# Optimization experiments

Measured on AMD Instinct MI355X. Metric: run time of the kernel, lower is better.

The kernel has to match this reference:

```python
import jax, jax.numpy as jnp
import numpy as np

B, S, E, H = 2, 2048, 2048, 16
D = E // H  # head_dim = 128
EPS = 1e-5


def setup_inputs() -> dict:
    key = jax.random.key(0)
    ks = jax.random.split(key, 16)
    s_e = 1.0 / np.sqrt(E)
    s_f = 1.0 / np.sqrt(4 * E)
    return {
        "x": jax.random.normal(ks[0], (B, S, E), jnp.float32),
        "ln1_w": jnp.ones((E,), jnp.float32) + 0.01 * jax.random.normal(ks[1], (E,)),
        "ln1_b": 0.01 * jax.random.normal(ks[2], (E,)),
        "wq": s_e * jax.random.normal(ks[3], (E, E), jnp.float32),
        "wk": s_e * jax.random.normal(ks[4], (E, E), jnp.float32),
        "wv": s_e * jax.random.normal(ks[5], (E, E), jnp.float32),
        "wo": s_e * jax.random.normal(ks[6], (E, E), jnp.float32),
        "bo": 0.01 * jax.random.normal(ks[7], (E,)),
        "ln2_w": jnp.ones((E,), jnp.float32) + 0.01 * jax.random.normal(ks[8], (E,)),
        "ln2_b": 0.01 * jax.random.normal(ks[9], (E,)),
        "w1": s_e * jax.random.normal(ks[10], (E, 4 * E), jnp.float32),
        "b1": 0.01 * jax.random.normal(ks[11], (4 * E,)),
        "w2": s_f * jax.random.normal(ks[12], (4 * E, E), jnp.float32),
        "b2": 0.01 * jax.random.normal(ks[13], (E,)),
    }


def _layernorm(x, w, b):
    mu = jnp.mean(x, axis=-1, keepdims=True)
    var = jnp.var(x, axis=-1, keepdims=True)
    return (x - mu) * jax.lax.rsqrt(var + EPS) * w + b


def _attention(x, wq, wk, wv, wo, bo):
    # x: [B,S,E] -> q,k,v: [B,H,S,D]
    def split(t):
        return t.reshape(B, S, H, D).transpose(0, 2, 1, 3)
    q = split(x @ wq)
    k = split(x @ wk)
    v = split(x @ wv)
    scores = jnp.einsum("bhqd,bhkd->bhqk", q, k)  # [B,H,S,S]
    causal = jnp.triu(jnp.ones((S, S), bool), k=1)
    scores = jnp.where(causal, -jnp.inf, scores)
    # NOTE: faithful to source -- scaling applied after masking, inside softmax arg
    attn = jax.nn.softmax(scores / np.sqrt(D), axis=-1)
    ctx = jnp.einsum("bhqk,bhkd->bhqd", attn, v)
    ctx = ctx.transpose(0, 2, 1, 3).reshape(B, S, E)
    return ctx @ wo + bo


def reference(x, ln1_w, ln1_b, wq, wk, wv, wo, bo, ln2_w, ln2_b, w1, b1, w2, b2):
    shortcut = x
    x1 = _layernorm(x, ln1_w, ln1_b)
    attn_out = _attention(x1, wq, wk, wv, wo, bo)
    a = attn_out + shortcut
    # NOTE: faithful to source quirk -- second shortcut is post-LN1 x1, not a
    y = _layernorm(a, ln2_w, ln2_b)
    y = jax.nn.gelu(y @ w1 + b1, approximate=False) @ w2 + b2
    return x1 + y
```

## Files before the change

### kernel.cpp

```cpp
#include <hip/hip_runtime.h>
#include <math.h>

typedef unsigned short u16;
typedef unsigned int u32;
typedef __attribute__((ext_vector_type(8))) short short8;
typedef __attribute__((ext_vector_type(4))) float f32x4;
typedef __attribute__((ext_vector_type(16))) float f32x16;
typedef __attribute__((ext_vector_type(4))) u32 u32x4;
typedef __attribute__((ext_vector_type(2))) u32 u32x2;

#define DEVFN static __device__ __forceinline__

DEVFN u16 f2bf(float x) {
  union { float f; u32 u; } v; v.f = x;
  u32 r = v.u + 0x7fffu + ((v.u >> 16) & 1u);
  return (u16)(r >> 16);
}
DEVFN float bf2f(u16 h) {
  union { u32 u; float f; } v; v.u = ((u32)h) << 16;
  return v.f;
}
DEVFN u32 packbf2(float a, float b) {
  return (u32)f2bf(a) | ((u32)f2bf(b) << 16);
}
DEVFN void gl2lds16(const u16* g, u16* l) {
  __builtin_amdgcn_global_load_lds(
      (const __attribute__((address_space(1))) u32*)g,
      (__attribute__((address_space(3))) u32*)l, 16, 0, 0);
}

__global__ __launch_bounds__(256) void tconv_k(const float* __restrict__ in,
                                               u16* __restrict__ out, int K, int N) {
  __shared__ float tile[32][33];
  int n0 = blockIdx.x << 5, k0 = blockIdx.y << 5;
  int tx = threadIdx.x & 31, ty = threadIdx.x >> 5;
#pragma unroll
  for (int i = 0; i < 32; i += 8)
    tile[ty + i][tx] = in[(long)(k0 + ty + i) * N + n0 + tx];
  __syncthreads();
#pragma unroll
  for (int i = 0; i < 32; i += 8)
    out[(long)(n0 + ty + i) * K + k0 + tx] = f2bf(tile[tx][ty + i]);
}

__global__ __launch_bounds__(256) void ln1_k(const float* __restrict__ x,
                                             const float* __restrict__ w,
                                             const float* __restrict__ b,
                                             float* __restrict__ y32,
                                             u16* __restrict__ y16) {
  long base = (long)blockIdx.x * 2048;
  int t = threadIdx.x;
  float4 v0 = ((const float4*)(x + base))[2 * t];
  float4 v1 = ((const float4*)(x + base))[2 * t + 1];
  float xv[8];
  *(float4*)xv = v0; *(float4*)(xv + 4) = v1;
  float s = 0.f, ss = 0.f;
#pragma unroll
  for (int i = 0; i < 8; ++i) { s += xv[i]; ss += xv[i] * xv[i]; }
#pragma unroll
  for (int m = 1; m < 64; m <<= 1) { s += __shfl_xor(s, m); ss += __shfl_xor(ss, m); }
  __shared__ float rs[4], rss[4];
  int wave = t >> 6;
  if ((t & 63) == 0) { rs[wave] = s; rss[wave] = ss; }
  __syncthreads();
  s = rs[0] + rs[1] + rs[2] + rs[3];
  ss = rss[0] + rss[1] + rss[2] + rss[3];
  float mean = s * (1.f / 2048.f);
  float var = ss * (1.f / 2048.f) - mean * mean;
  float inv = rsqrtf(var + 1e-5f);
  float wv[8], bv[8];
  *(float4*)wv = ((const float4*)w)[2 * t]; *(float4*)(wv + 4) = ((const float4*)w)[2 * t + 1];
  *(float4*)bv = ((const float4*)b)[2 * t]; *(float4*)(bv + 4) = ((const float4*)b)[2 * t + 1];
  float yv[8];
#pragma unroll
  for (int i = 0; i < 8; ++i) yv[i] = (xv[i] - mean) * inv * wv[i] + bv[i];
  ((float4*)(y32 + base))[2 * t] = *(float4*)yv;
  ((float4*)(y32 + base))[2 * t + 1] = *(float4*)(yv + 4);
  u32x4 ov;
#pragma unroll
  for (int i = 0; i < 4; ++i) ov[i] = packbf2(yv[2 * i], yv[2 * i + 1]);
  ((u32x4*)(y16 + base))[t] = ov;
}

__global__ __launch_bounds__(256) void ln2_k(const u16* __restrict__ a,
                                             const float* __restrict__ w,
                                             const float* __restrict__ b,
                                             u16* __restrict__ y) {
  long base = (long)blockIdx.x * 2048;
  int t = threadIdx.x;
  u32x4 pv = ((const u32x4*)(a + base))[t];
  float xv[8];
#pragma unroll
  for (int i = 0; i < 4; ++i) {
    xv[2 * i] = bf2f((u16)(pv[i] & 0xffffu));
    xv[2 * i + 1] = bf2f((u16)(pv[i] >> 16));
  }
  float s = 0.f, ss = 0.f;
#pragma unroll
  for (int i = 0; i < 8; ++i) { s += xv[i]; ss += xv[i] * xv[i]; }
#pragma unroll
  for (int m = 1; m < 64; m <<= 1) { s += __shfl_xor(s, m); ss += __shfl_xor(ss, m); }
  __shared__ float rs[4], rss[4];
  int wave = t >> 6;
  if ((t & 63) == 0) { rs[wave] = s; rss[wave] = ss; }
  __syncthreads();
  s = rs[0] + rs[1] + rs[2] + rs[3];
  ss = rss[0] + rss[1] + rss[2] + rss[3];
  float mean = s * (1.f / 2048.f);
  float var = ss * (1.f / 2048.f) - mean * mean;
  float inv = rsqrtf(var + 1e-5f);
  float wv[8], bv[8];
  *(float4*)wv = ((const float4*)w)[2 * t]; *(float4*)(wv + 4) = ((const float4*)w)[2 * t + 1];
  *(float4*)bv = ((const float4*)b)[2 * t]; *(float4*)(bv + 4) = ((const float4*)b)[2 * t + 1];
  u32x4 ov;
#pragma unroll
  for (int i = 0; i < 4; ++i) {
    float y0 = (xv[2 * i] - mean) * inv * wv[2 * i] + bv[2 * i];
    float y1 = (xv[2 * i + 1] - mean) * inv * wv[2 * i + 1] + bv[2 * i + 1];
    ov[i] = packbf2(y0, y1);
  }
  ((u32x4*)(y + base))[t] = ov;
}

#define VMW4() asm volatile("s_waitcnt vmcnt(4)" ::: "memory")
#define VMW2() asm volatile("s_waitcnt vmcnt(2)" ::: "memory")
#define VMW0() asm volatile("s_waitcnt vmcnt(0)" ::: "memory")
#define CFENCE() asm volatile("" ::: "memory")
#define BARRIER() do { CFENCE(); __builtin_amdgcn_s_barrier(); CFENCE(); } while (0)

template <int MODE, int IM>
__global__ __launch_bounds__(512, 2) void gemm8_k(const u16* __restrict__ A,
                                                  const u16* __restrict__ W,
                                                  void* __restrict__ outp,
                                                  const float* __restrict__ bias,
                                                  const float* __restrict__ resid,
                                                  int M, int N, int K) {
  constexpr int BM = IM * 32;
  constexpr int BN = 256;
  __shared__ __align__(16) u16 lds[2][(BM + BN) * 64];
  const int t = threadIdx.x, lane = t & 63, wave = t >> 6;
  const int g = lane >> 4, r16 = lane & 15;
  const int wm = wave >> 2, wn = wave & 3;
  const int nM = M / BM;
  const int nwg = gridDim.x * gridDim.y;
  const int orig = blockIdx.y * gridDim.x + blockIdx.x;
  const int sw = (nwg & 7) ? orig : ((orig & 7) * (nwg >> 3) + (orig >> 3));
  const long m0 = (long)(sw % nM) * BM, n0 = (long)(sw / nM) * BN;
  const int nt = K >> 6;
  const long Kl = K;

  auto stA = [&](int b, int half, int tile) {
#pragma unroll
    for (int q = 0; q < 2; ++q) {
      int rl = (wave * 2 + q) * 8 + (lane >> 3);
      int c = (lane & 7) ^ (rl & 7);
      gl2lds16(A + (m0 + half * 128 + rl) * Kl + ((long)tile << 6) + c * 8,
               &lds[b][half * 8192 + (wave * 2 + q) * 512]);
    }
  };
  auto stB = [&](int b, int half, int tile) {
#pragma unroll
    for (int q = 0; q < 2; ++q) {
      int rl = (wave * 2 + q) * 8 + (lane >> 3);
      int c = (lane & 7) ^ (rl & 7);
      gl2lds16(W + (n0 + half * 128 + rl) * Kl + ((long)tile << 6) + c * 8,
               &lds[b][BM * 64 + half * 8192 + (wave * 2 + q) * 512]);
    }
  };

  f32x4 acc[IM][4] = {};
  short8 af[4][2], bf[2][2];

#define LDAF(IH)                                                              \
  _Pragma("unroll") for (int ii2 = 0; ii2 < 4; ++ii2) {                       \
    int row = (((IH)*4 + ii2) * 2 + wm) * 16 + r16;                           \
    _Pragma("unroll") for (int kk = 0; kk < 2; ++kk)                          \
        af[ii2][kk] = *(const short8*)(&lds[cur][row * 64 +                   \
                                        (((kk << 2) | g) ^ (row & 7)) * 8]);  \
  }
#define LDBF(JH)                                                              \
  _Pragma("unroll") for (int jj2 = 0; jj2 < 2; ++jj2) {                       \
    int row = (((JH)*2 + jj2) * 4 + wn) * 16 + r16;                           \
    _Pragma("unroll") for (int kk = 0; kk < 2; ++kk)                          \
        bf[jj2][kk] = *(const short8*)(&lds[cur][BM * 64 + row * 64 +         \
                                        (((kk << 2) | g) ^ (row & 7)) * 8]);  \
  }
#define MFMA_PH(IH, JH)                                                       \
  __builtin_amdgcn_s_setprio(1);                                              \
  _Pragma("unroll") for (int ii2 = 0; ii2 < 4; ++ii2)                         \
      _Pragma("unroll") for (int jj2 = 0; jj2 < 2; ++jj2)                     \
          _Pragma("unroll") for (int kk = 0; kk < 2; ++kk)                    \
              acc[(IH)*4 + ii2][(JH)*2 + jj2] =                               \
                  __builtin_amdgcn_mfma_f32_16x16x32_bf16(                    \
                      af[ii2][kk], bf[jj2][kk],                               \
                      acc[(IH)*4 + ii2][(JH)*2 + jj2], 0, 0, 0);              \
  __builtin_amdgcn_s_setprio(0);

  if constexpr (IM == 8) {
    stA(0, 0, 0); stB(0, 0, 0); stB(0, 1, 0); stA(0, 1, 0);
    VMW4();
  } else {
    stA(0, 0, 0); stB(0, 0, 0); stB(0, 1, 0);
    VMW2();
  }
  BARRIER();

  for (int tt = 0; tt < nt; ++tt) {
    const int cur = tt & 1, nxt = cur ^ 1;
    const int ts = (tt + 1 < nt) ? tt + 1 : tt;
    if constexpr (IM == 8) {
      LDAF(0); LDBF(0);
      stA(nxt, 0, ts);
      MFMA_PH(0, 0);
      VMW4(); BARRIER();
      LDBF(1);
      stB(nxt, 0, ts);
      MFMA_PH(0, 1);
      VMW4(); BARRIER();
      LDAF(1); LDBF(0);
      stB(nxt, 1, ts);
      MFMA_PH(1, 0);
      BARRIER();
      LDBF(1);
      stA(nxt, 1, ts);
      MFMA_PH(1, 1);
      VMW4(); BARRIER();
    } else {
      LDAF(0); LDBF(0);
      stA(nxt, 0, ts); stB(nxt, 0, ts);
      MFMA_PH(0, 0);
      VMW4(); BARRIER();
      LDBF(1);
      stB(nxt, 1, ts);
      MFMA_PH(0, 1);
      VMW2(); BARRIER();
    }
  }
  VMW0();

  const long Nl = N;
#pragma unroll
  for (int ii = 0; ii < IM; ++ii) {
#pragma unroll
    for (int jj = 0; jj < 4; ++jj) {
#pragma unroll
      for (int r = 0; r < 4; ++r) {
        long mg = m0 + (ii * 2 + wm) * 16 + g * 4 + r;
        long ng = n0 + (jj * 4 + wn) * 16 + r16;
        float v = acc[ii][jj][r];
        if constexpr (MODE == 0 || MODE == 1) {
          long bb = mg >> 11, sq = mg & 2047;
          long hh = ng >> 7, dd = ng & 127;
          long idx = (MODE == 0) ? (((bb * 16 + hh) * 2048 + sq) * 128 + dd)
                                 : (((bb * 16 + hh) * 128 + dd) * 2048 + sq);
          ((u16*)outp)[idx] = f2bf(v);
        } else if constexpr (MODE == 2) {
          v += bias[ng] + resid[mg * Nl + ng];
          ((u16*)outp)[mg * Nl + ng] = f2bf(v);
        } else if constexpr (MODE == 3) {
          v += bias[ng];
          v = 0.5f * v * (1.0f + erff(v * 0.70710678118654752f));
          ((u16*)outp)[mg * Nl + ng] = f2bf(v);
        } else {
          v += bias[ng] + resid[mg * Nl + ng];
          ((float*)outp)[mg * Nl + ng] = v;
        }
      }
    }
  }
#undef LDAF
#undef LDBF
#undef MFMA_PH
}

__global__ __launch_bounds__(256, 2) void attn2_k(const u16* __restrict__ Qp,
                                                  const u16* __restrict__ Kp,
                                                  const u16* __restrict__ Vp,
                                                  u16* __restrict__ ctx) {
  __shared__ __align__(16) u16 KsL[2][64 * 128];
  __shared__ __align__(16) u16 VsL[2][128 * 64];
  const int qt = gridDim.x - 1 - blockIdx.x;
  const int bh = blockIdx.y;
  const int t = threadIdx.x, lane = t & 63, wave = t >> 6;
  const int l31 = lane & 31, hi = lane >> 5;
  const int q0 = qt * 128, qw0 = q0 + wave * 32;
  const int qg = qw0 + l31;
  const u16* Qh = Qp + (long)bh * 2048 * 128;
  const u16* Kh = Kp + (long)bh * 2048 * 128;
  const u16* Vh = Vp + (long)bh * 128 * 2048;
  const int nkt = qt * 2 + 2;
  const int ktmax = (qw0 + 31) >> 6;
  const float cs = 0.12753042923810058f;

  short8 qf[8];
#pragma unroll
  for (int ds = 0; ds < 8; ++ds)
    qf[ds] = *(const short8*)(Qh + (long)qg * 128 + ds * 16 + hi * 8);

  f32x16 O0 = {}, O1 = {}, O2 = {}, O3 = {};
  float m = -INFINITY, l = 0.f;

  auto stage = [&](int b, int kt) {
#pragma unroll
    for (int q = 0; q < 4; ++q) {
      int r = wave * 16 + q * 4 + (lane >> 4);
      int c = (lane & 15) ^ (r & 15);
      gl2lds16(Kh + ((long)kt * 64 + r) * 128 + c * 8,
               &KsL[b][(wave * 16 + q * 4) * 128]);
    }
#pragma unroll
    for (int q = 0; q < 4; ++q) {
      int r = wave * 32 + q * 8 + (lane >> 3);
      int c = (lane & 7) ^ (r & 7);
      gl2lds16(Vh + (long)r * 2048 + kt * 64 + c * 8,
               &VsL[b][(wave * 32 + q * 8) * 64]);
    }
  };

  stage(0, 0);
  VMW0(); BARRIER();

  for (int kt = 0; kt < nkt; ++kt) {
    const int cur = kt & 1;
    if (kt + 1 < nkt) stage(cur ^ 1, kt + 1);
    if (kt <= ktmax) {
      f32x16 S0 = {}, S1 = {};
      __builtin_amdgcn_s_setprio(1);
#pragma unroll
      for (int ds = 0; ds < 8; ++ds) {
        int c0 = ((ds * 2 + hi) ^ (l31 & 15)) * 8;
        short8 k0 = *(const short8*)(&KsL[cur][l31 * 128 + c0]);
        int r1 = 32 + l31;
        int c1 = ((ds * 2 + hi) ^ (r1 & 15)) * 8;
        short8 k1 = *(const short8*)(&KsL[cur][r1 * 128 + c1]);
        S0 = __builtin_amdgcn_mfma_f32_32x32x16_bf16(k0, qf[ds], S0, 0, 0, 0);
        S1 = __builtin_amdgcn_mfma_f32_32x32x16_bf16(k1, qf[ds], S1, 0, 0, 0);
      }
      __builtin_amdgcn_s_setprio(0);
      float p[32];
#pragma unroll
      for (int i = 0; i < 16; ++i) { p[i] = S0[i]; p[16 + i] = S1[i]; }
      if (kt * 64 + 63 > qw0) {
#pragma unroll
        for (int ks = 0; ks < 2; ++ks)
#pragma unroll
          for (int r = 0; r < 16; ++r) {
            int kg = kt * 64 + ks * 32 + (r & 3) + 8 * (r >> 2) + 4 * hi;
            if (kg > qg) p[ks * 16 + r] = -INFINITY;
          }
      }
      float tmax = p[0];
#pragma unroll
      for (int i = 1; i < 32; ++i) tmax = fmaxf(tmax, p[i]);
      tmax = fmaxf(tmax, __shfl_xor(tmax, 32));
      float mnew = fmaxf(m, tmax);
      float corr = __builtin_amdgcn_exp2f((m - mnew) * cs);
      float ls = 0.f;
#pragma unroll
      for (int i = 0; i < 32; ++i) {
        p[i] = __builtin_amdgcn_exp2f((p[i] - mnew) * cs);
        ls += p[i];
      }
      ls += __shfl_xor(ls, 32);
      l = l * corr + ls;
      m = mnew;
#pragma unroll
      for (int i = 0; i < 16; ++i) {
        O0[i] *= corr; O1[i] *= corr; O2[i] *= corr; O3[i] *= corr;
      }
      short8 pf[4];
#pragma unroll
      for (int gg = 0; gg < 4; ++gg) {
        u32 u_, v_, w_, z_;
        asm("v_cvt_pk_bf16_f32 %0, %1, %2" : "=v"(u_) : "v"(p[gg * 8 + 0]), "v"(p[gg * 8 + 1]));
        asm("v_cvt_pk_bf16_f32 %0, %1, %2" : "=v"(v_) : "v"(p[gg * 8 + 2]), "v"(p[gg * 8 + 3]));
        asm("v_cvt_pk_bf16_f32 %0, %1, %2" : "=v"(w_) : "v"(p[gg * 8 + 4]), "v"(p[gg * 8 + 5]));
        asm("v_cvt_pk_bf16_f32 %0, %1, %2" : "=v"(z_) : "v"(p[gg * 8 + 6]), "v"(p[gg * 8 + 7]));
        asm("v_permlane32_swap_b32 %0, %1" : "+v"(u_), "+v"(w_));
        asm("v_permlane32_swap_b32 %0, %1" : "+v"(v_), "+v"(z_));
        union { u32 w4[4]; short8 s; } cv;
        cv.w4[0] = u_; cv.w4[1] = v_; cv.w4[2] = w_; cv.w4[3] = z_;
        pf[gg] = cv.s;
      }
      __builtin_amdgcn_s_setprio(1);
#define PVROW(ds, OO)                                                          \
  {                                                                            \
    int row = (ds)*32 + l31;                                                   \
    _Pragma("unroll") for (int gg = 0; gg < 4; ++gg) {                         \
      short8 vf = *(const short8*)(&VsL[cur][row * 64 +                        \
                                             (((gg * 2 + hi) ^ (row & 7)) * 8)]); \
      OO = __builtin_amdgcn_mfma_f32_32x32x16_bf16(vf, pf[gg], OO, 0, 0, 0);   \
    }                                                                          \
  }
      PVROW(0, O0); PVROW(1, O1); PVROW(2, O2); PVROW(3, O3);
#undef PVROW
      __builtin_amdgcn_s_setprio(0);
    }
    VMW0(); BARRIER();
  }

  const float inv = 1.f / l;
  u16* cp = ctx + ((long)(bh >> 4) * 2048 + qg) * 2048 + (bh & 15) * 128;
#define WROUT(OO, dsb)                                                         \
  _Pragma("unroll") for (int rg = 0; rg < 4; ++rg) {                           \
    int d = (dsb)*32 + 8 * rg + 4 * hi;                                        \
    u32x2 wv;                                                                  \
    wv[0] = packbf2(OO[4 * rg] * inv, OO[4 * rg + 1] * inv);                   \
    wv[1] = packbf2(OO[4 * rg + 2] * inv, OO[4 * rg + 3] * inv);               \
    *(u32x2*)(cp + d) = wv;                                                    \
  }
  WROUT(O0, 0); WROUT(O1, 1); WROUT(O2, 2); WROUT(O3, 3);
#undef WROUT
}

extern "C" void kernel_launch(void* const* d_in, const int* in_sizes, int n_in,
                              void* d_out, int out_size, void* d_ws, size_t ws_size,
                              hipStream_t stream) {
  const float* x = (const float*)d_in[0];
  const float* ln1w = (const float*)d_in[1];
  const float* ln1b = (const float*)d_in[2];
  const float* wq = (const float*)d_in[3];
  const float* wk = (const float*)d_in[4];
  const float* wv = (const float*)d_in[5];
  const float* wo = (const float*)d_in[6];
  const float* bo = (const float*)d_in[7];
  const float* ln2w = (const float*)d_in[8];
  const float* ln2b = (const float*)d_in[9];
  const float* w1 = (const float*)d_in[10];
  const float* b1 = (const float*)d_in[11];
  const float* w2 = (const float*)d_in[12];
  const float* b2 = (const float*)d_in[13];
  float* out = (float*)d_out;
  char* ws = (char*)d_ws;

  float* x1f = (float*)(ws + 0);
  u16* x1b = (u16*)(ws + 33554432);
  u16* wqt = (u16*)(ws + 50331648);
  u16* wkt = (u16*)(ws + 58720256);
  u16* wvt = (u16*)(ws + 67108864);
  u16* wot = (u16*)(ws + 75497472);
  u16* w1t = (u16*)(ws + 83886080);
  u16* w2t = (u16*)(ws + 117440512);
  u16* qb = (u16*)(ws + 150994944);
  u16* kb = (u16*)(ws + 167772160);
  u16* vb = (u16*)(ws + 184549376);
  u16* ctxb = (u16*)(ws + 201326592);
  u16* ab = (u16*)(ws + 218103808);
  u16* y0b = (u16*)(ws + 234881024);
  u16* hb = qb;

  tconv_k<<<dim3(64, 64), 256, 0, stream>>>(wq, wqt, 2048, 2048);
  tconv_k<<<dim3(64, 64), 256, 0, stream>>>(wk, wkt, 2048, 2048);
  tconv_k<<<dim3(64, 64), 256, 0, stream>>>(wv, wvt, 2048, 2048);
  tconv_k<<<dim3(64, 64), 256, 0, stream>>>(wo, wot, 2048, 2048);
  tconv_k<<<dim3(256, 64), 256, 0, stream>>>(w1, w1t, 2048, 8192);
  tconv_k<<<dim3(64, 256), 256, 0, stream>>>(w2, w2t, 8192, 2048);
  ln1_k<<<4096, 256, 0, stream>>>(x, ln1w, ln1b, x1f, x1b);
  gemm8_k<0, 4><<<dim3(32, 8), 512, 0, stream>>>(x1b, wqt, qb, nullptr, nullptr, 4096, 2048, 2048);
  gemm8_k<0, 4><<<dim3(32, 8), 512, 0, stream>>>(x1b, wkt, kb, nullptr, nullptr, 4096, 2048, 2048);
  gemm8_k<1, 4><<<dim3(32, 8), 512, 0, stream>>>(x1b, wvt, vb, nullptr, nullptr, 4096, 2048, 2048);
  attn2_k<<<dim3(16, 32), 256, 0, stream>>>(qb, kb, vb, ctxb);
  gemm8_k<2, 4><<<dim3(32, 8), 512, 0, stream>>>(ctxb, wot, ab, bo, x, 4096, 2048, 2048);
  ln2_k<<<4096, 256, 0, stream>>>(ab, ln2w, ln2b, y0b);
  gemm8_k<3, 8><<<dim3(16, 32), 512, 0, stream>>>(y0b, w1t, hb, b1, nullptr, 4096, 8192, 2048);
  gemm8_k<4, 4><<<dim3(32, 8), 512, 0, stream>>>(hb, w2t, out, b2, x1f, 4096, 2048, 8192);
}
```

Measured before the change: 669.0 us.

## Triple-buffer GEMM pipeline, fuse QKV projections, and use polynomial GELU

Replaces the double-buffered 128/256-row GEMM with a single 128x256 tile kernel that uses three LDS buffers, prefetching two K-tiles ahead. The Q, K and V projections become one launch over a concatenated N=6144 weight, with the epilogue routing each column to its destination layout. The FC1 GEMM now uses 128-row tiles instead of 256. GELU's erff is replaced by an Abramowitz-Stegun polynomial with fast exp and reciprocal. The extra LDS buffer may lower occupancy, and the erf approximation adds a small error.

```diff
diff --git a/kernel.cpp b/kernel.cpp
--- a/kernel.cpp
+++ b/kernel.cpp
@@ -27,6 +27,19 @@
   __builtin_amdgcn_global_load_lds(
       (const __attribute__((address_space(1))) u32*)g,
       (__attribute__((address_space(3))) u32*)l, 16, 0, 0);
+}
+DEVFN float gelu_exact(float v) {
+  float s = v * 0.70710678118654752f;
+  float ax = fabsf(s);
+  float t = __builtin_amdgcn_rcpf(1.0f + 0.3275911f * ax);
+  float poly = t * (0.254829592f +
+               t * (-0.284496736f +
+               t * (1.421413741f +
+               t * (-1.453152027f + t * 1.061405429f))));
+  float e = __expf(-s * s);
+  float er = 1.0f - poly * e;
+  er = (s < 0.f) ? -er : er;
+  return 0.5f * v * (1.0f + er);
 }
 
 __global__ __launch_bounds__(256) void tconv_k(const float* __restrict__ in,
@@ -122,125 +135,114 @@
   ((u32x4*)(y + base))[t] = ov;
 }
 
-#define VMW4() asm volatile("s_waitcnt vmcnt(4)" ::: "memory")
-#define VMW2() asm volatile("s_waitcnt vmcnt(2)" ::: "memory")
+#define VMW6() asm volatile("s_waitcnt vmcnt(6)" ::: "memory")
 #define VMW0() asm volatile("s_waitcnt vmcnt(0)" ::: "memory")
 #define CFENCE() asm volatile("" ::: "memory")
 #define BARRIER() do { CFENCE(); __builtin_amdgcn_s_barrier(); CFENCE(); } while (0)
 
-template <int MODE, int IM>
-__global__ __launch_bounds__(512, 2) void gemm8_k(const u16* __restrict__ A,
+template <int MODE>
+__global__ __launch_bounds__(512, 2) void gemm3_k(const u16* __restrict__ A,
                                                   const u16* __restrict__ W,
                                                   void* __restrict__ outp,
                                                   const float* __restrict__ bias,
                                                   const float* __restrict__ resid,
                                                   int M, int N, int K) {
-  constexpr int BM = IM * 32;
-  constexpr int BN = 256;
-  __shared__ __align__(16) u16 lds[2][(BM + BN) * 64];
+  __shared__ __align__(16) u16 lds[3][24576];
   const int t = threadIdx.x, lane = t & 63, wave = t >> 6;
   const int g = lane >> 4, r16 = lane & 15;
   const int wm = wave >> 2, wn = wave & 3;
-  const int nM = M / BM;
+  const int nM = M >> 7;
   const int nwg = gridDim.x * gridDim.y;
   const int orig = blockIdx.y * gridDim.x + blockIdx.x;
   const int sw = (nwg & 7) ? orig : ((orig & 7) * (nwg >> 3) + (orig >> 3));
-  const long m0 = (long)(sw % nM) * BM, n0 = (long)(sw / nM) * BN;
+  const long m0 = (long)(sw % nM) * 128, n0 = (long)(sw / nM) * 256;
   const int nt = K >> 6;
   const long Kl = K;
-
-  auto stA = [&](int b, int half, int tile) {
+  const int rl = lane >> 3, cc = lane & 7;
+
+  auto stA = [&](u16* Lb, long tile) {
 #pragma unroll
     for (int q = 0; q < 2; ++q) {
-      int rl = (wave * 2 + q) * 8 + (lane >> 3);
-      int c = (lane & 7) ^ (rl & 7);
-      gl2lds16(A + (m0 + half * 128 + rl) * Kl + ((long)tile << 6) + c * 8,
-               &lds[b][half * 8192 + (wave * 2 + q) * 512]);
+      int rr = (wave * 2 + q) * 8 + rl;
+      int c = cc ^ (rr & 7);
+      gl2lds16(A + (m0 + rr) * Kl + (tile << 6) + c * 8, Lb + (wave * 2 + q) * 512);
     }
   };
-  auto stB = [&](int b, int half, int tile) {
+  auto stB = [&](u16* Lb, int half, long tile) {
 #pragma unroll
     for (int q = 0; q < 2; ++q) {
-      int rl = (wave * 2 + q) * 8 + (lane >> 3);
-      int c = (lane & 7) ^ (rl & 7);
-      gl2lds16(W + (n0 + half * 128 + rl) * Kl + ((long)tile << 6) + c * 8,
-               &lds[b][BM * 64 + half * 8192 + (wave * 2 + q) * 512]);
+      int rr = (wave * 2 + q) * 8 + rl;
+      int c = cc ^ (rr & 7);
+      gl2lds16(W + (n0 + half * 128 + rr) * Kl + (tile << 6) + c * 8,
+               Lb + 8192 + half * 8192 + (wave * 2 + q) * 512);
     }
   };
 
-  f32x4 acc[IM][4] = {};
-  short8 af[4][2], bf[2][2];
-
-#define LDAF(IH)                                                              \
-  _Pragma("unroll") for (int ii2 = 0; ii2 < 4; ++ii2) {                       \
-    int row = (((IH)*4 + ii2) * 2 + wm) * 16 + r16;                           \
-    _Pragma("unroll") for (int kk = 0; kk < 2; ++kk)                          \
-        af[ii2][kk] = *(const short8*)(&lds[cur][row * 64 +                   \
-                                        (((kk << 2) | g) ^ (row & 7)) * 8]);  \
-  }
-#define LDBF(JH)                                                              \
-  _Pragma("unroll") for (int jj2 = 0; jj2 < 2; ++jj2) {                       \
-    int row = (((JH)*2 + jj2) * 4 + wn) * 16 + r16;                           \
-    _Pragma("unroll") for (int kk = 0; kk < 2; ++kk)                          \
-        bf[jj2][kk] = *(const short8*)(&lds[cur][BM * 64 + row * 64 +         \
-                                        (((kk << 2) | g) ^ (row & 7)) * 8]);  \
-  }
-#define MFMA_PH(IH, JH)                                                       \
-  __builtin_amdgcn_s_setprio(1);                                              \
-  _Pragma("unroll") for (int ii2 = 0; ii2 < 4; ++ii2)                         \
-      _Pragma("unroll") for (int jj2 = 0; jj2 < 2; ++jj2)                     \
-          _Pragma("unroll") for (int kk = 0; kk < 2; ++kk)                    \
-              acc[(IH)*4 + ii2][(JH)*2 + jj2] =                               \
-                  __builtin_amdgcn_mfma_f32_16x16x32_bf16(                    \
-                      af[ii2][kk], bf[jj2][kk],                               \
-                      acc[(IH)*4 + ii2][(JH)*2 + jj2], 0, 0, 0);              \
-  __builtin_amdgcn_s_setprio(0);
-
-  if constexpr (IM == 8) {
-    stA(0, 0, 0); stB(0, 0, 0); stB(0, 1, 0); stA(0, 1, 0);
-    VMW4();
-  } else {
-    stA(0, 0, 0); stB(0, 0, 0); stB(0, 1, 0);
-    VMW2();
-  }
+  f32x4 acc[4][4] = {};
+  u16* L0 = &lds[0][0];
+  u16* L1 = &lds[1][0];
+  u16* L2 = &lds[2][0];
+
+  stA(L0, 0); stB(L0, 0, 0); stB(L0, 1, 0);
+  if (nt > 1) { stA(L1, 1); stB(L1, 0, 1); stB(L1, 1, 1); }
+  if (nt > 2) { VMW6(); } else { VMW0(); }
   BARRIER();
 
   for (int tt = 0; tt < nt; ++tt) {
-    const int cur = tt & 1, nxt = cur ^ 1;
-    const int ts = (tt + 1 < nt) ? tt + 1 : tt;
-    if constexpr (IM == 8) {
-      LDAF(0); LDBF(0);
-      stA(nxt, 0, ts);
-      MFMA_PH(0, 0);
-      VMW4(); BARRIER();
-      LDBF(1);
-      stB(nxt, 0, ts);
-      MFMA_PH(0, 1);
-      VMW4(); BARRIER();
-      LDAF(1); LDBF(0);
-      stB(nxt, 1, ts);
-      MFMA_PH(1, 0);
-      BARRIER();
-      LDBF(1);
-      stA(nxt, 1, ts);
-      MFMA_PH(1, 1);
-      VMW4(); BARRIER();
-    } else {
-      LDAF(0); LDBF(0);
-      stA(nxt, 0, ts); stB(nxt, 0, ts);
-      MFMA_PH(0, 0);
-      VMW4(); BARRIER();
-      LDBF(1);
-      stB(nxt, 1, ts);
-      MFMA_PH(0, 1);
-      VMW2(); BARRIER();
-    }
+    const long ts = (tt + 2 < nt) ? (long)(tt + 2) : (long)(nt - 1);
+    short8 af[4][2], bf[2][2];
+#pragma unroll
+    for (int ii2 = 0; ii2 < 4; ++ii2) {
+      int row = (ii2 * 2 + wm) * 16 + r16;
+#pragma unroll
+      for (int kk = 0; kk < 2; ++kk)
+        af[ii2][kk] = *(const short8*)(L0 + row * 64 + (((kk << 2) | g) ^ (row & 7)) * 8);
+    }
+#pragma unroll
+    for (int jj2 = 0; jj2 < 2; ++jj2) {
+      int row = (jj2 * 4 + wn) * 16 + r16;
+#pragma unroll
+      for (int kk = 0; kk < 2; ++kk)
+        bf[jj2][kk] = *(const short8*)(L0 + 8192 + row * 64 + (((kk << 2) | g) ^ (row & 7)) * 8);
+    }
+    stA(L2, ts); stB(L2, 0, ts);
+    __builtin_amdgcn_s_setprio(1);
+#pragma unroll
+    for (int ii2 = 0; ii2 < 4; ++ii2)
+#pragma unroll
+      for (int jj2 = 0; jj2 < 2; ++jj2)
+#pragma unroll
+        for (int kk = 0; kk < 2; ++kk)
+          acc[ii2][jj2] = __builtin_amdgcn_mfma_f32_16x16x32_bf16(
+              af[ii2][kk], bf[jj2][kk], acc[ii2][jj2], 0, 0, 0);
+    __builtin_amdgcn_s_setprio(0);
+    BARRIER();
+#pragma unroll
+    for (int jj2 = 0; jj2 < 2; ++jj2) {
+      int row = ((2 + jj2) * 4 + wn) * 16 + r16;
+#pragma unroll
+      for (int kk = 0; kk < 2; ++kk)
+        bf[jj2][kk] = *(const short8*)(L0 + 8192 + row * 64 + (((kk << 2) | g) ^ (row & 7)) * 8);
+    }
+    stB(L2, 1, ts);
+    __builtin_amdgcn_s_setprio(1);
+#pragma unroll
+    for (int ii2 = 0; ii2 < 4; ++ii2)
+#pragma unroll
+      for (int jj2 = 0; jj2 < 2; ++jj2)
+#pragma unroll
+        for (int kk = 0; kk < 2; ++kk)
+          acc[ii2][2 + jj2] = __builtin_amdgcn_mfma_f32_16x16x32_bf16(
+              af[ii2][kk], bf[jj2][kk], acc[ii2][2 + jj2], 0, 0, 0);
+    __builtin_amdgcn_s_setprio(0);
+    VMW6(); BARRIER();
+    u16* tmp = L0; L0 = L1; L1 = L2; L2 = tmp;
   }
   VMW0();
 
   const long Nl = N;
 #pragma unroll
-  for (int ii = 0; ii < IM; ++ii) {
+  for (int ii = 0; ii < 4; ++ii) {
 #pragma unroll
     for (int jj = 0; jj < 4; ++jj) {
 #pragma unroll
@@ -248,18 +250,19 @@
         long mg = m0 + (ii * 2 + wm) * 16 + g * 4 + r;
         long ng = n0 + (jj * 4 + wn) * 16 + r16;
         float v = acc[ii][jj][r];
-        if constexpr (MODE == 0 || MODE == 1) {
+        if constexpr (MODE == 0) {
+          int which = (int)(n0 >> 11);
+          long nloc = ng & 2047;
           long bb = mg >> 11, sq = mg & 2047;
-          long hh = ng >> 7, dd = ng & 127;
-          long idx = (MODE == 0) ? (((bb * 16 + hh) * 2048 + sq) * 128 + dd)
+          long hh = nloc >> 7, dd = nloc & 127;
+          long idx = (which < 2) ? (((bb * 16 + hh) * 2048 + sq) * 128 + dd)
                                  : (((bb * 16 + hh) * 128 + dd) * 2048 + sq);
-          ((u16*)outp)[idx] = f2bf(v);
+          ((u16*)outp)[(long)which * 8388608 + idx] = f2bf(v);
         } else if constexpr (MODE == 2) {
           v += bias[ng] + resid[mg * Nl + ng];
           ((u16*)outp)[mg * Nl + ng] = f2bf(v);
         } else if constexpr (MODE == 3) {
-          v += bias[ng];
-          v = 0.5f * v * (1.0f + erff(v * 0.70710678118654752f));
+          v = gelu_exact(v + bias[ng]);
           ((u16*)outp)[mg * Nl + ng] = f2bf(v);
         } else {
           v += bias[ng] + resid[mg * Nl + ng];
@@ -268,9 +271,6 @@
       }
     }
   }
-#undef LDAF
-#undef LDBF
-#undef MFMA_PH
 }
 
 __global__ __launch_bounds__(256, 2) void attn2_k(const u16* __restrict__ Qp,
@@ -456,12 +456,10 @@
   tconv_k<<<dim3(256, 64), 256, 0, stream>>>(w1, w1t, 2048, 8192);
   tconv_k<<<dim3(64, 256), 256, 0, stream>>>(w2, w2t, 8192, 2048);
   ln1_k<<<4096, 256, 0, stream>>>(x, ln1w, ln1b, x1f, x1b);
-  gemm8_k<0, 4><<<dim3(32, 8), 512, 0, stream>>>(x1b, wqt, qb, nullptr, nullptr, 4096, 2048, 2048);
-  gemm8_k<0, 4><<<dim3(32, 8), 512, 0, stream>>>(x1b, wkt, kb, nullptr, nullptr, 4096, 2048, 2048);
-  gemm8_k<1, 4><<<dim3(32, 8), 512, 0, stream>>>(x1b, wvt, vb, nullptr, nullptr, 4096, 2048, 2048);
+  gemm3_k<0><<<dim3(32, 24), 512, 0, stream>>>(x1b, wqt, qb, nullptr, nullptr, 4096, 6144, 2048);
   attn2_k<<<dim3(16, 32), 256, 0, stream>>>(qb, kb, vb, ctxb);
-  gemm8_k<2, 4><<<dim3(32, 8), 512, 0, stream>>>(ctxb, wot, ab, bo, x, 4096, 2048, 2048);
+  gemm3_k<2><<<dim3(32, 8), 512, 0, stream>>>(ctxb, wot, ab, bo, x, 4096, 2048, 2048);
   ln2_k<<<4096, 256, 0, stream>>>(ab, ln2w, ln2b, y0b);
-  gemm8_k<3, 8><<<dim3(16, 32), 512, 0, stream>>>(y0b, w1t, hb, b1, nullptr, 4096, 8192, 2048);
-  gemm8_k<4, 4><<<dim3(32, 8), 512, 0, stream>>>(hb, w2t, out, b2, x1f, 4096, 2048, 8192);
-}
+  gemm3_k<3><<<dim3(32, 32), 512, 0, stream>>>(y0b, w1t, hb, b1, nullptr, 4096, 8192, 2048);
+  gemm3_k<4><<<dim3(32, 8), 512, 0, stream>>>(hb, w2t, out, b2, x1f, 4096, 2048, 8192);
+}
```

New measurement: 664.8 us. No clear change (-0.6%).

## Fuse weight transposes, merge QKV GEMMs, and use polynomial GELU

Applied to the files above, without the earlier changes.

Merges the six weight-transpose launches into a single kernel that dispatches on block index. The three Q/K/V projection GEMMs become one N=6144 GEMM with a larger M tile, relying on wqt/wkt/wvt and qb/kb/vb sitting contiguously in the workspace, and per-column logic picks the Q/K vs V output layout. GELU's erff is replaced with an Abramowitz-Stegun polynomial using a fast reciprocal and exp, which reduces epilogue cost at some accuracy loss (about 1e-7 absolute error in erf). These changes aim to cut launch overhead, raise GEMM occupancy and reuse, and speed up the FFN epilogue.

```diff
diff --git a/kernel.cpp b/kernel.cpp
--- a/kernel.cpp
+++ b/kernel.cpp
@@ -28,11 +28,49 @@
       (const __attribute__((address_space(1))) u32*)g,
       (__attribute__((address_space(3))) u32*)l, 16, 0, 0);
 }
-
-__global__ __launch_bounds__(256) void tconv_k(const float* __restrict__ in,
-                                               u16* __restrict__ out, int K, int N) {
+DEVFN float gelu_exact(float v) {
+  float s = v * 0.70710678118654752f;
+  float ax = fabsf(s);
+  float t = __builtin_amdgcn_rcpf(1.0f + 0.3275911f * ax);
+  float poly = t * (0.254829592f +
+               t * (-0.284496736f +
+               t * (1.421413741f +
+               t * (-1.453152027f + t * 1.061405429f))));
+  float e = __expf(-s * s);
+  float er = 1.0f - poly * e;
+  er = (s < 0.f) ? -er : er;
+  return 0.5f * v * (1.0f + er);
+}
+
+#define VMW4() asm volatile("s_waitcnt vmcnt(4)" ::: "memory")
+#define VMW2() asm volatile("s_waitcnt vmcnt(2)" ::: "memory")
+#define VMW0() asm volatile("s_waitcnt vmcnt(0)" ::: "memory")
+#define CFENCE() asm volatile("" ::: "memory")
+#define BARRIER() do { CFENCE(); __builtin_amdgcn_s_barrier(); CFENCE(); } while (0)
+
+__global__ __launch_bounds__(256) void tconvall_k(
+    const float* __restrict__ wq, const float* __restrict__ wk,
+    const float* __restrict__ wv, const float* __restrict__ wo,
+    const float* __restrict__ w1, const float* __restrict__ w2,
+    u16* __restrict__ wqt, u16* __restrict__ wkt, u16* __restrict__ wvt,
+    u16* __restrict__ wot, u16* __restrict__ w1t, u16* __restrict__ w2t) {
   __shared__ float tile[32][33];
-  int n0 = blockIdx.x << 5, k0 = blockIdx.y << 5;
+  int b = blockIdx.x;
+  const float* in; u16* out; int K, N, tn, tk;
+  if (b < 16384) {
+    int wsel = b >> 12;
+    int loc = b & 4095;
+    in = (wsel == 0) ? wq : (wsel == 1) ? wk : (wsel == 2) ? wv : wo;
+    out = (wsel == 0) ? wqt : (wsel == 1) ? wkt : (wsel == 2) ? wvt : wot;
+    K = 2048; N = 2048; tn = loc & 63; tk = loc >> 6;
+  } else if (b < 32768) {
+    int loc = b - 16384; in = w1; out = w1t; K = 2048; N = 8192;
+    tn = loc & 255; tk = loc >> 8;
+  } else {
+    int loc = b - 32768; in = w2; out = w2t; K = 8192; N = 2048;
+    tn = loc & 63; tk = loc >> 6;
+  }
+  int n0 = tn << 5, k0 = tk << 5;
   int tx = threadIdx.x & 31, ty = threadIdx.x >> 5;
 #pragma unroll
   for (int i = 0; i < 32; i += 8)
@@ -121,12 +159,6 @@
   }
   ((u32x4*)(y + base))[t] = ov;
 }
-
-#define VMW4() asm volatile("s_waitcnt vmcnt(4)" ::: "memory")
-#define VMW2() asm volatile("s_waitcnt vmcnt(2)" ::: "memory")
-#define VMW0() asm volatile("s_waitcnt vmcnt(0)" ::: "memory")
-#define CFENCE() asm volatile("" ::: "memory")
-#define BARRIER() do { CFENCE(); __builtin_amdgcn_s_barrier(); CFENCE(); } while (0)
 
 template <int MODE, int IM>
 __global__ __launch_bounds__(512, 2) void gemm8_k(const u16* __restrict__ A,
@@ -248,18 +280,19 @@
         long mg = m0 + (ii * 2 + wm) * 16 + g * 4 + r;
         long ng = n0 + (jj * 4 + wn) * 16 + r16;
         float v = acc[ii][jj][r];
-        if constexpr (MODE == 0 || MODE == 1) {
+        if constexpr (MODE == 0) {
+          long which = ng >> 11;
+          long nloc = ng & 2047;
           long bb = mg >> 11, sq = mg & 2047;
-          long hh = ng >> 7, dd = ng & 127;
-          long idx = (MODE == 0) ? (((bb * 16 + hh) * 2048 + sq) * 128 + dd)
+          long hh = nloc >> 7, dd = nloc & 127;
+          long idx = (which < 2) ? (((bb * 16 + hh) * 2048 + sq) * 128 + dd)
                                  : (((bb * 16 + hh) * 128 + dd) * 2048 + sq);
-          ((u16*)outp)[idx] = f2bf(v);
+          ((u16*)outp)[which * 8388608 + idx] = f2bf(v);
         } else if constexpr (MODE == 2) {
           v += bias[ng] + resid[mg * Nl + ng];
           ((u16*)outp)[mg * Nl + ng] = f2bf(v);
         } else if constexpr (MODE == 3) {
-          v += bias[ng];
-          v = 0.5f * v * (1.0f + erff(v * 0.70710678118654752f));
+          v = gelu_exact(v + bias[ng]);
           ((u16*)outp)[mg * Nl + ng] = f2bf(v);
         } else {
           v += bias[ng] + resid[mg * Nl + ng];
@@ -449,16 +482,10 @@
   u16* y0b = (u16*)(ws + 234881024);
   u16* hb = qb;
 
-  tconv_k<<<dim3(64, 64), 256, 0, stream>>>(wq, wqt, 2048, 2048);
-  tconv_k<<<dim3(64, 64), 256, 0, stream>>>(wk, wkt, 2048, 2048);
-  tconv_k<<<dim3(64, 64), 256, 0, stream>>>(wv, wvt, 2048, 2048);
-  tconv_k<<<dim3(64, 64), 256, 0, stream>>>(wo, wot, 2048, 2048);
-  tconv_k<<<dim3(256, 64), 256, 0, stream>>>(w1, w1t, 2048, 8192);
-  tconv_k<<<dim3(64, 256), 256, 0, stream>>>(w2, w2t, 8192, 2048);
+  tconvall_k<<<49152, 256, 0, stream>>>(wq, wk, wv, wo, w1, w2,
+                                        wqt, wkt, wvt, wot, w1t, w2t);
   ln1_k<<<4096, 256, 0, stream>>>(x, ln1w, ln1b, x1f, x1b);
-  gemm8_k<0, 4><<<dim3(32, 8), 512, 0, stream>>>(x1b, wqt, qb, nullptr, nullptr, 4096, 2048, 2048);
-  gemm8_k<0, 4><<<dim3(32, 8), 512, 0, stream>>>(x1b, wkt, kb, nullptr, nullptr, 4096, 2048, 2048);
-  gemm8_k<1, 4><<<dim3(32, 8), 512, 0, stream>>>(x1b, wvt, vb, nullptr, nullptr, 4096, 2048, 2048);
+  gemm8_k<0, 8><<<dim3(16, 24), 512, 0, stream>>>(x1b, wqt, qb, nullptr, nullptr, 4096, 6144, 2048);
   attn2_k<<<dim3(16, 32), 256, 0, stream>>>(qb, kb, vb, ctxb);
   gemm8_k<2, 4><<<dim3(32, 8), 512, 0, stream>>>(ctxb, wot, ab, bo, x, 4096, 2048, 2048);
   ln2_k<<<4096, 256, 0, stream>>>(ab, ln2w, ln2b, y0b);
```

Measured after the change: 661.0 us. Within noise of the previous version (-1.2%).
